# Kernel tuning notes

Hardware: AMD Instinct MI355X
Metric: run time of the kernel (lower is better)

The kernel has to match this reference:

```python
import jax, jax.numpy as jnp
import numpy as np

GEN_DIM = 200
CON_DIM = 128
CO_DIM = 4
LATENT_DIM = 64
CI_ENC_DIM = 128
EXT_DIM = 16
CLIP = 5.0
B = 65536

GEN_IN = EXT_DIM + CO_DIM            # 20
CON_IN = 2 * CI_ENC_DIM + LATENT_DIM # 320
STATE_DIM = GEN_DIM + CON_DIM + CO_DIM + CO_DIM + (CO_DIM + EXT_DIM) + LATENT_DIM  # 420


def _gru_cell(x, h, w_ih, w_hh, b_ih, b_hh, clip):
    # torch GRUCell convention: gates ordered (r, z, n), hidden clipped (LFADS ClippedGRUCell)
    gi = x @ w_ih.T + b_ih
    gh = h @ w_hh.T + b_hh
    i_r, i_z, i_n = jnp.split(gi, 3, axis=1)
    h_r, h_z, h_n = jnp.split(gh, 3, axis=1)
    r = jax.nn.sigmoid(i_r + h_r)
    z = jax.nn.sigmoid(i_z + h_z)
    n = jnp.tanh(i_n + r * h_n)
    h_new = (1.0 - z) * n + z * h
    return jnp.clip(h_new, -clip, clip)


def setup_inputs() -> dict:
    key = jax.random.key(0)
    ks = jax.random.split(key, 14)
    def w(k, shape, fan_in):
        return (jax.random.normal(k, shape, jnp.float32) / np.sqrt(fan_in)).astype(jnp.float32)
    return {
        "x": jax.random.normal(ks[0], (B, 2 * CI_ENC_DIM + EXT_DIM), jnp.float32),
        "h0": jax.random.normal(ks[1], (B, STATE_DIM), jnp.float32),
        "eps": jax.random.normal(ks[2], (B, CO_DIM), jnp.float32),
        "gen_w_ih": w(ks[3], (3 * GEN_DIM, GEN_IN), GEN_IN),
        "gen_w_hh": w(ks[4], (3 * GEN_DIM, GEN_DIM), GEN_DIM),
        "gen_b_ih": jnp.zeros((3 * GEN_DIM,), jnp.float32),
        "gen_b_hh": jnp.zeros((3 * GEN_DIM,), jnp.float32),
        "con_w_ih": w(ks[5], (3 * CON_DIM, CON_IN), CON_IN),
        "con_w_hh": w(ks[6], (3 * CON_DIM, CON_DIM), CON_DIM),
        "con_b_ih": jnp.zeros((3 * CON_DIM,), jnp.float32),
        "con_b_hh": jnp.zeros((3 * CON_DIM,), jnp.float32),
        "co_w": w(ks[7], (2 * CO_DIM, CON_DIM), CON_DIM),
        "co_b": jnp.zeros((2 * CO_DIM,), jnp.float32),
        "fac_w": w(ks[8], (LATENT_DIM, GEN_DIM), GEN_DIM),
    }


def reference(x, h0, eps, gen_w_ih, gen_w_hh, gen_b_ih, gen_b_hh,
              con_w_ih, con_w_hh, con_b_ih, con_b_hh, co_w, co_b, fac_w):
    # split h0 per state_dims [GEN, CON, CO, CO, CO+EXT, LATENT]
    o0 = GEN_DIM
    o1 = o0 + CON_DIM
    o2 = o1 + CO_DIM
    o3 = o2 + CO_DIM
    o4 = o3 + CO_DIM + EXT_DIM
    gen_state = h0[:, :o0]
    con_state = h0[:, o0:o1]
    factor = h0[:, o4:]
    # split input per [2*CI_ENC_DIM, EXT_DIM]
    ci_step = x[:, :2 * CI_ENC_DIM]
    ext_step = x[:, 2 * CI_ENC_DIM:]

    # controller path (dropout is identity at inference)
    con_input = jnp.concatenate([ci_step, factor], axis=1)
    con_state = _gru_cell(con_input, con_state, con_w_ih, con_w_hh, con_b_ih, con_b_hh, CLIP)
    co_params = con_state @ co_w.T + co_b
    co_mean = co_params[:, :CO_DIM]
    co_logvar = co_params[:, CO_DIM:]
    co_std = jnp.exp(0.5 * co_logvar)  # sqrt(exp(logvar))
    con_output = co_mean + co_std * eps  # reparameterized rsample

    gen_input = jnp.concatenate([con_output, ext_step], axis=1)
    gen_state = _gru_cell(gen_input, gen_state, gen_w_ih, gen_w_hh, gen_b_ih, gen_b_hh, CLIP)

    # kernel-normalized linear: rows L2-normalized, no bias
    normed_w = fac_w / jnp.maximum(jnp.linalg.norm(fac_w, axis=1, keepdims=True), 1e-12)
    factor = gen_state @ normed_w.T

    hidden = jnp.concatenate([gen_state, con_state, co_mean, co_std, gen_input, factor], axis=1)
    return hidden
```

## Files before the change

### kernel.cpp

```cpp
#include <hip/hip_runtime.h>
#include <math.h>


#define NT 512
#define RT 128
#define XD 272
#define HD 420

typedef unsigned short ushort_t;
typedef __attribute__((ext_vector_type(8))) short bf8;
typedef __attribute__((ext_vector_type(4))) float f4;
typedef __attribute__((ext_vector_type(4))) unsigned short us4;

#define WS_W1 0
#define WS_W2 122880
#define WS_W3 172032
#define WS_W4 191488
#define WS_W5 327680

#define STA 328
#define STG 216
#define STH 136
#define STR3 88

#define O_A   0
#define O_GN  55296
#define O_R2  83968
#define O_R3  118784
#define POOLB 141312

__device__ __forceinline__ ushort_t f2bf(float f) {
  union { float f; unsigned u; } v; v.f = f;
  unsigned r = v.u + 0x7FFFu + ((v.u >> 16) & 1u);
  return (ushort_t)(r >> 16);
}
__device__ __forceinline__ float bf2f(ushort_t u) {
  union { unsigned u; float f; } v; v.u = ((unsigned)u) << 16; return v.f;
}
__device__ __forceinline__ us4 f2bf4(f4 v) {
  us4 b; b.x = f2bf(v.x); b.y = f2bf(v.y); b.z = f2bf(v.z); b.w = f2bf(v.w); return b;
}
__device__ __forceinline__ f4 bf2f4(us4 b) {
  f4 v; v.x = bf2f(b.x); v.y = bf2f(b.y); v.z = bf2f(b.z); v.w = bf2f(b.w); return v;
}
__device__ __forceinline__ float rcpf(float x) { return __builtin_amdgcn_rcpf(x); }
__device__ __forceinline__ float sigf(float x) { return rcpf(1.0f + __expf(-x)); }
__device__ __forceinline__ float tanhf_(float x) {
  return 1.0f - 2.0f * rcpf(1.0f + __expf(2.0f * x));
}

#define MFMA(a, b, c) __builtin_amdgcn_mfma_f32_16x16x32_bf16((a), (b), (c), 0, 0, 0)

__global__ void prep_w(const float* __restrict__ cw1, const float* __restrict__ cw2,
                       const float* __restrict__ gw3, const float* __restrict__ gw4,
                       ushort_t* __restrict__ ws) {
  int tid = blockIdx.x * blockDim.x + threadIdx.x;
  int np = gridDim.x * blockDim.x;
  for (int i = tid; i < 384 * 320; i += np) ws[WS_W1 + i] = f2bf(cw1[i]);
  for (int i = tid; i < 384 * 128; i += np) ws[WS_W2 + i] = f2bf(cw2[i]);
  for (int i = tid; i < 608 * 32; i += np) {
    int n = i >> 5, k = i & 31;
    ws[WS_W3 + i] = (n < 600 && k < 20) ? f2bf(gw3[n * 20 + k]) : (ushort_t)0;
  }
  for (int i = tid; i < 608 * 224; i += np) {
    int n = i / 224, k = i - n * 224;
    ws[WS_W4 + i] = (n < 600 && k < 200) ? f2bf(gw4[n * 200 + k]) : (ushort_t)0;
  }
}

__global__ void prep_fac(const float* __restrict__ fw, ushort_t* __restrict__ ws) {
  int n = blockIdx.x;
  int l = threadIdx.x;
  float ss = 0.f;
  for (int k = l; k < 200; k += 64) { float v = fw[n * 200 + k]; ss = fmaf(v, v, ss); }
  for (int off = 32; off; off >>= 1) ss += __shfl_down(ss, off, 64);
  ss = __shfl(ss, 0, 64);
  float inv = 1.0f / fmaxf(sqrtf(ss), 1e-12f);
  for (int k = l; k < 224; k += 64)
    ws[WS_W5 + n * 224 + k] = (k < 200) ? f2bf(fw[n * 200 + k] * inv) : (ushort_t)0;
}

__global__ __launch_bounds__(NT, 2) void decoder_kernel(
    const float* __restrict__ x, const float* __restrict__ h0, const float* __restrict__ eps,
    const float* __restrict__ gen_b_ih, const float* __restrict__ gen_b_hh,
    const float* __restrict__ con_b_ih, const float* __restrict__ con_b_hh,
    const float* __restrict__ co_w, const float* __restrict__ co_b,
    const ushort_t* __restrict__ ws, float* __restrict__ out)
{
  __shared__ __align__(16) unsigned char spool[POOLB];
  ushort_t* sA  = (ushort_t*)(spool + O_A);
  ushort_t* sGo = (ushort_t*)(spool + O_A);
  ushort_t* sGn = (ushort_t*)(spool + O_GN);
  ushort_t* sR2 = (ushort_t*)(spool + O_R2);
  ushort_t* sR3 = (ushort_t*)(spool + O_R3);

  const int tid = threadIdx.x;
  const int rbase = blockIdx.x * RT;
  const int lane = tid & 63;
  const int w = tid >> 6;
  const int bn = lane & 15;
  const int kq = (lane >> 4) << 3;
  const int qrow = (lane >> 4) << 2;

  #pragma unroll
  for (int it = 0; it < 16; ++it) {
    int idx = tid + it * NT;
    int r = idx >> 6, c4 = (idx & 63) << 2;
    f4 v = *(const f4*)&x[(size_t)(rbase + r) * XD + c4];
    *(us4*)&sA[r * STA + c4] = f2bf4(v);
  }
  {
    int r = tid >> 2, e = (tid & 3) << 2;
    f4 v = *(const f4*)&x[(size_t)(rbase + r) * XD + 256 + e];
    *(us4*)&sR3[r * STR3 + 4 + e] = f2bf4(v);
    *(f4*)&out[(size_t)(rbase + r) * HD + 340 + e] = v;
  }
  #pragma unroll
  for (int it = 0; it < 8; ++it) {
    int idx = tid + it * NT;
    int r = idx >> 5, c4 = (idx & 31) << 2;
    f4 v = *(const f4*)&h0[(size_t)(rbase + r) * HD + 200 + c4];
    *(us4*)&sR2[r * STH + c4] = f2bf4(v);
  }
  #pragma unroll
  for (int it = 0; it < 4; ++it) {
    int idx = tid + it * NT;
    int r = idx >> 4, c4 = (idx & 15) << 2;
    f4 v = *(const f4*)&h0[(size_t)(rbase + r) * HD + 356 + c4];
    *(us4*)&sA[r * STA + 256 + c4] = f2bf4(v);
  }
  if (tid < 384) {
    int r = tid / 3, q = (tid - (tid / 3) * 3) << 2;
    us4 z = {0, 0, 0, 0};
    *(us4*)&sR3[r * STR3 + 20 + q] = z;
  }
  __syncthreads();

  const int col = (w << 4) + bn;

  f4 aR[8], aZ[8], aN[8], aHN[8];
  #pragma unroll
  for (int ri = 0; ri < 8; ++ri) {
    aR[ri] = (f4){0.f, 0.f, 0.f, 0.f};
    aZ[ri] = (f4){0.f, 0.f, 0.f, 0.f};
    aN[ri] = (f4){0.f, 0.f, 0.f, 0.f};
    aHN[ri] = (f4){0.f, 0.f, 0.f, 0.f};
  }
  {
    const ushort_t* W2 = ws + WS_W2;
    #pragma unroll 1
    for (int k0 = 0; k0 < 128; k0 += 32) {
      bf8 b0 = *(const bf8*)&W2[(size_t)(col) * 128 + k0 + kq];
      bf8 b1 = *(const bf8*)&W2[(size_t)(128 + col) * 128 + k0 + kq];
      bf8 bm = *(const bf8*)&W2[(size_t)(256 + col) * 128 + k0 + kq];
      #pragma unroll
      for (int ri = 0; ri < 8; ++ri) {
        bf8 a = *(const bf8*)&sR2[(ri * 16 + bn) * STH + k0 + kq];
        aR[ri] = MFMA(a, b0, aR[ri]);
        aZ[ri] = MFMA(a, b1, aZ[ri]);
        aHN[ri] = MFMA(a, bm, aHN[ri]);
      }
    }
    const ushort_t* W1 = ws + WS_W1;
    #pragma unroll 1
    for (int k0 = 0; k0 < 320; k0 += 32) {
      bf8 b0 = *(const bf8*)&W1[(size_t)(col) * 320 + k0 + kq];
      bf8 b1 = *(const bf8*)&W1[(size_t)(128 + col) * 320 + k0 + kq];
      bf8 bm = *(const bf8*)&W1[(size_t)(256 + col) * 320 + k0 + kq];
      #pragma unroll
      for (int ri = 0; ri < 8; ++ri) {
        bf8 a = *(const bf8*)&sA[(ri * 16 + bn) * STA + k0 + kq];
        aR[ri] = MFMA(a, b0, aR[ri]);
        aZ[ri] = MFMA(a, b1, aZ[ri]);
        aN[ri] = MFMA(a, bm, aN[ri]);
      }
    }
  }
  __syncthreads();

  #pragma unroll 1
  for (int idx = tid; idx < 128 * 54; idx += NT) {
    int r = idx / 54, u = idx - (idx / 54) * 54;
    if (u < 50) {
      f4 v = *(const f4*)&h0[(size_t)(rbase + r) * HD + (u << 2)];
      *(us4*)&sGo[r * STG + (u << 2)] = f2bf4(v);
    } else {
      us4 z = {0, 0, 0, 0};
      *(us4*)&sGo[r * STG + 200 + ((u - 50) << 2)] = z;
    }
  }
  {
    float brr = con_b_ih[col] + con_b_hh[col];
    float brz = con_b_ih[128 + col] + con_b_hh[128 + col];
    float bin = con_b_ih[256 + col], bhn = con_b_hh[256 + col];
    #pragma unroll
    for (int ri = 0; ri < 8; ++ri) {
      #pragma unroll
      for (int j = 0; j < 4; ++j) {
        int row = ri * 16 + qrow + j;
        float hold = bf2f(sR2[row * STH + col]);
        float rr = sigf(aR[ri][j] + brr);
        float zz = sigf(aZ[ri][j] + brz);
        float nn = tanhf_(aN[ri][j] + bin + rr * (aHN[ri][j] + bhn));
        float hv = (1.f - zz) * nn + zz * hold;
        hv = fminf(fmaxf(hv, -5.f), 5.f);
        sR2[row * STH + col] = f2bf(hv);
        out[(size_t)(rbase + row) * HD + 200 + col] = hv;
      }
    }
  }
  __syncthreads();

  {
    int cn = tid & 7;
    #pragma unroll
    for (int half = 0; half < 2; ++half) {
      int crow = (tid >> 3) + half * 64;
      float acc = co_b[cn];
      #pragma unroll 8
      for (int k0 = 0; k0 < 128; k0 += 4) {
        f4 hv = bf2f4(*(const us4*)&sR2[crow * STH + k0]);
        f4 wv = *(const f4*)&co_w[cn * 128 + k0];
        acc = fmaf(hv.x, wv.x, acc);
        acc = fmaf(hv.y, wv.y, acc);
        acc = fmaf(hv.z, wv.z, acc);
        acc = fmaf(hv.w, wv.w, acc);
      }
      float lv = __shfl(acc, lane + 4, 64);
      if (cn < 4) {
        float stdv = __expf(0.5f * lv);
        float ov = fmaf(stdv, eps[(size_t)(rbase + crow) * 4 + cn], acc);
        size_t orow = (size_t)(rbase + crow) * HD;
        out[orow + 328 + cn] = acc;
        out[orow + 332 + cn] = stdv;
        out[orow + 336 + cn] = ov;
        sR3[crow * STR3 + cn] = f2bf(ov);
      }
    }
  }
  __syncthreads();

  {
    int r = tid >> 2, q = (tid & 3) << 2;
    us4 z = {0, 0, 0, 0};
    *(us4*)&sGn[r * STG + 200 + q] = z;
  }
  {
    const ushort_t* W3 = ws + WS_W3;
    const ushort_t* W4 = ws + WS_W4;
    #pragma unroll 1
    for (int t = w; t < 13; t += 8) {
      int c = (t << 4) + bn;
      f4 gR[8], gZ[8], gN[8], gHN[8];
      #pragma unroll
      for (int ri = 0; ri < 8; ++ri) {
        gR[ri] = (f4){0.f, 0.f, 0.f, 0.f};
        gZ[ri] = (f4){0.f, 0.f, 0.f, 0.f};
        gN[ri] = (f4){0.f, 0.f, 0.f, 0.f};
        gHN[ri] = (f4){0.f, 0.f, 0.f, 0.f};
      }
      {
        bf8 b0 = *(const bf8*)&W3[(size_t)(c) * 32 + kq];
        bf8 b1 = *(const bf8*)&W3[(size_t)(200 + c) * 32 + kq];
        bf8 bm = *(const bf8*)&W3[(size_t)(400 + c) * 32 + kq];
        #pragma unroll
        for (int ri = 0; ri < 8; ++ri) {
          bf8 a = *(const bf8*)&sR3[(ri * 16 + bn) * STR3 + kq];
          gR[ri] = MFMA(a, b0, gR[ri]);
          gZ[ri] = MFMA(a, b1, gZ[ri]);
          gN[ri] = MFMA(a, bm, gN[ri]);
        }
      }
      #pragma unroll 1
      for (int k0 = 0; k0 < 224; k0 += 32) {
        bf8 b0 = *(const bf8*)&W4[(size_t)(c) * 224 + k0 + kq];
        bf8 b1 = *(const bf8*)&W4[(size_t)(200 + c) * 224 + k0 + kq];
        bf8 bm = *(const bf8*)&W4[(size_t)(400 + c) * 224 + k0 + kq];
        #pragma unroll
        for (int ri = 0; ri < 8; ++ri) {
          bf8 a = *(const bf8*)&sGo[(ri * 16 + bn) * STG + k0 + kq];
          gR[ri] = MFMA(a, b0, gR[ri]);
          gZ[ri] = MFMA(a, b1, gZ[ri]);
          gHN[ri] = MFMA(a, bm, gHN[ri]);
        }
      }
      if (c < 200) {
        float brr = gen_b_ih[c] + gen_b_hh[c];
        float brz = gen_b_ih[200 + c] + gen_b_hh[200 + c];
        float bin = gen_b_ih[400 + c], bhn = gen_b_hh[400 + c];
        #pragma unroll
        for (int ri = 0; ri < 8; ++ri) {
          #pragma unroll
          for (int j = 0; j < 4; ++j) {
            int row = ri * 16 + qrow + j;
            float hold = bf2f(sGo[row * STG + c]);
            float rr = sigf(gR[ri][j] + brr);
            float zz = sigf(gZ[ri][j] + brz);
            float nn = tanhf_(gN[ri][j] + bin + rr * (gHN[ri][j] + bhn));
            float hv = (1.f - zz) * nn + zz * hold;
            hv = fminf(fmaxf(hv, -5.f), 5.f);
            sGn[row * STG + c] = f2bf(hv);
            out[(size_t)(rbase + row) * HD + c] = hv;
          }
        }
      }
    }
  }
  __syncthreads();

  {
    const ushort_t* W5 = ws + WS_W5;
    #pragma unroll 1
    for (int job = 0; job < 4; ++job) {
      int ri = ((w & 3) << 1) + (job & 1);
      int ct = ((w >> 2) << 1) + (job >> 1);
      bf8 w5f[7];
      #pragma unroll
      for (int k = 0; k < 7; ++k)
        w5f[k] = *(const bf8*)&W5[(size_t)((ct << 4) + bn) * 224 + k * 32 + kq];
      f4 acc = (f4){0.f, 0.f, 0.f, 0.f};
      #pragma unroll
      for (int k = 0; k < 7; ++k) {
        bf8 a = *(const bf8*)&sGn[(ri * 16 + bn) * STG + k * 32 + kq];
        acc = MFMA(a, w5f[k], acc);
      }
      #pragma unroll
      for (int j = 0; j < 4; ++j) {
        int row = ri * 16 + qrow + j;
        out[(size_t)(rbase + row) * HD + 356 + (ct << 4) + bn] = acc[j];
      }
    }
  }
}

extern "C" void kernel_launch(void* const* d_in, const int* in_sizes, int n_in,
                              void* d_out, int out_size, void* d_ws, size_t ws_size,
                              hipStream_t stream) {
  const float* x        = (const float*)d_in[0];
  const float* h0       = (const float*)d_in[1];
  const float* eps      = (const float*)d_in[2];
  const float* gen_w_ih = (const float*)d_in[3];
  const float* gen_w_hh = (const float*)d_in[4];
  const float* gen_b_ih = (const float*)d_in[5];
  const float* gen_b_hh = (const float*)d_in[6];
  const float* con_w_ih = (const float*)d_in[7];
  const float* con_w_hh = (const float*)d_in[8];
  const float* con_b_ih = (const float*)d_in[9];
  const float* con_b_hh = (const float*)d_in[10];
  const float* co_w     = (const float*)d_in[11];
  const float* co_b     = (const float*)d_in[12];
  const float* fac_w    = (const float*)d_in[13];
  float* out = (float*)d_out;
  ushort_t* ws = (ushort_t*)d_ws;

  hipLaunchKernelGGL(prep_w, dim3(256), dim3(512), 0, stream,
                     con_w_ih, con_w_hh, gen_w_ih, gen_w_hh, ws);
  hipLaunchKernelGGL(prep_fac, dim3(64), dim3(64), 0, stream, fac_w, ws);

  int nrows = in_sizes[2] / 4;
  int grid = nrows / RT;
  hipLaunchKernelGGL(decoder_kernel, dim3(grid), dim3(NT), 0, stream,
                     x, h0, eps, gen_b_ih, gen_b_hh, con_b_ih, con_b_hh,
                     co_w, co_b, ws, out);
}
```

Before: 155.0 us.

## Split fused decoder into separate controller and generator kernels with 32-row tiles

Splits the single fused decoder kernel into a controller kernel and a generator kernel. The generator reads the controller output back from the output buffer in global memory. Row tiles shrink from 128 to 32 and blocks from 512 to 256 threads, which cuts shared memory per block and raises occupancy and grid size. In exchange, each weight fragment loaded from global or L2 now feeds only two row tiles instead of eight, so weight traffic per row rises. There is also an extra kernel launch and a global round trip for the generator input.

```diff
diff --git a/kernel.cpp b/kernel.cpp
--- a/kernel.cpp
+++ b/kernel.cpp
@@ -2,8 +2,6 @@
 #include <math.h>
 
 
-#define NT 512
-#define RT 128
 #define XD 272
 #define HD 420
 
@@ -21,13 +19,6 @@
 #define STA 328
 #define STG 216
 #define STH 136
-#define STR3 88
-
-#define O_A   0
-#define O_GN  55296
-#define O_R2  83968
-#define O_R3  118784
-#define POOLB 141312
 
 __device__ __forceinline__ ushort_t f2bf(float f) {
   union { float f; unsigned u; } v; v.f = f;
@@ -80,22 +71,19 @@
     ws[WS_W5 + n * 224 + k] = (k < 200) ? f2bf(fw[n * 200 + k] * inv) : (ushort_t)0;
 }
 
-__global__ __launch_bounds__(NT, 2) void decoder_kernel(
-    const float* __restrict__ x, const float* __restrict__ h0, const float* __restrict__ eps,
-    const float* __restrict__ gen_b_ih, const float* __restrict__ gen_b_hh,
+__global__ __launch_bounds__(256, 4) void con_kernel(
+    const float* __restrict__ x, const float* __restrict__ h0,
+    const float* __restrict__ eps,
     const float* __restrict__ con_b_ih, const float* __restrict__ con_b_hh,
     const float* __restrict__ co_w, const float* __restrict__ co_b,
     const ushort_t* __restrict__ ws, float* __restrict__ out)
 {
-  __shared__ __align__(16) unsigned char spool[POOLB];
-  ushort_t* sA  = (ushort_t*)(spool + O_A);
-  ushort_t* sGo = (ushort_t*)(spool + O_A);
-  ushort_t* sGn = (ushort_t*)(spool + O_GN);
-  ushort_t* sR2 = (ushort_t*)(spool + O_R2);
-  ushort_t* sR3 = (ushort_t*)(spool + O_R3);
+  __shared__ __align__(16) unsigned char spool[29696];
+  ushort_t* sA  = (ushort_t*)(spool);
+  ushort_t* sR2 = (ushort_t*)(spool + 20992);
 
   const int tid = threadIdx.x;
-  const int rbase = blockIdx.x * RT;
+  const int rbase = blockIdx.x * 32;
   const int lane = tid & 63;
   const int w = tid >> 6;
   const int bn = lane & 15;
@@ -103,83 +91,152 @@
   const int qrow = (lane >> 4) << 2;
 
   #pragma unroll
-  for (int it = 0; it < 16; ++it) {
-    int idx = tid + it * NT;
+  for (int it = 0; it < 8; ++it) {
+    int idx = tid + it * 256;
     int r = idx >> 6, c4 = (idx & 63) << 2;
     f4 v = *(const f4*)&x[(size_t)(rbase + r) * XD + c4];
     *(us4*)&sA[r * STA + c4] = f2bf4(v);
   }
-  {
+  if (tid < 128) {
     int r = tid >> 2, e = (tid & 3) << 2;
     f4 v = *(const f4*)&x[(size_t)(rbase + r) * XD + 256 + e];
-    *(us4*)&sR3[r * STR3 + 4 + e] = f2bf4(v);
     *(f4*)&out[(size_t)(rbase + r) * HD + 340 + e] = v;
   }
   #pragma unroll
-  for (int it = 0; it < 8; ++it) {
-    int idx = tid + it * NT;
+  for (int it = 0; it < 4; ++it) {
+    int idx = tid + it * 256;
     int r = idx >> 5, c4 = (idx & 31) << 2;
     f4 v = *(const f4*)&h0[(size_t)(rbase + r) * HD + 200 + c4];
     *(us4*)&sR2[r * STH + c4] = f2bf4(v);
   }
   #pragma unroll
-  for (int it = 0; it < 4; ++it) {
-    int idx = tid + it * NT;
+  for (int it = 0; it < 2; ++it) {
+    int idx = tid + it * 256;
     int r = idx >> 4, c4 = (idx & 15) << 2;
     f4 v = *(const f4*)&h0[(size_t)(rbase + r) * HD + 356 + c4];
     *(us4*)&sA[r * STA + 256 + c4] = f2bf4(v);
   }
-  if (tid < 384) {
-    int r = tid / 3, q = (tid - (tid / 3) * 3) << 2;
-    us4 z = {0, 0, 0, 0};
-    *(us4*)&sR3[r * STR3 + 20 + q] = z;
-  }
-  __syncthreads();
-
-  const int col = (w << 4) + bn;
-
-  f4 aR[8], aZ[8], aN[8], aHN[8];
-  #pragma unroll
-  for (int ri = 0; ri < 8; ++ri) {
-    aR[ri] = (f4){0.f, 0.f, 0.f, 0.f};
-    aZ[ri] = (f4){0.f, 0.f, 0.f, 0.f};
-    aN[ri] = (f4){0.f, 0.f, 0.f, 0.f};
-    aHN[ri] = (f4){0.f, 0.f, 0.f, 0.f};
-  }
-  {
+  __syncthreads();
+
+  f4 aR[2][2], aZ[2][2], aN[2][2], aHN[2][2];
+  #pragma unroll
+  for (int ti = 0; ti < 2; ++ti)
+    #pragma unroll
+    for (int rt = 0; rt < 2; ++rt) {
+      aR[ti][rt] = (f4){0.f, 0.f, 0.f, 0.f};
+      aZ[ti][rt] = (f4){0.f, 0.f, 0.f, 0.f};
+      aN[ti][rt] = (f4){0.f, 0.f, 0.f, 0.f};
+      aHN[ti][rt] = (f4){0.f, 0.f, 0.f, 0.f};
+    }
+  #pragma unroll
+  for (int ti = 0; ti < 2; ++ti) {
+    const int col = ((w + 4 * ti) << 4) + bn;
     const ushort_t* W2 = ws + WS_W2;
-    #pragma unroll 1
+    #pragma unroll
     for (int k0 = 0; k0 < 128; k0 += 32) {
       bf8 b0 = *(const bf8*)&W2[(size_t)(col) * 128 + k0 + kq];
       bf8 b1 = *(const bf8*)&W2[(size_t)(128 + col) * 128 + k0 + kq];
       bf8 bm = *(const bf8*)&W2[(size_t)(256 + col) * 128 + k0 + kq];
       #pragma unroll
-      for (int ri = 0; ri < 8; ++ri) {
-        bf8 a = *(const bf8*)&sR2[(ri * 16 + bn) * STH + k0 + kq];
-        aR[ri] = MFMA(a, b0, aR[ri]);
-        aZ[ri] = MFMA(a, b1, aZ[ri]);
-        aHN[ri] = MFMA(a, bm, aHN[ri]);
+      for (int rt = 0; rt < 2; ++rt) {
+        bf8 a = *(const bf8*)&sR2[(rt * 16 + bn) * STH + k0 + kq];
+        aR[ti][rt] = MFMA(a, b0, aR[ti][rt]);
+        aZ[ti][rt] = MFMA(a, b1, aZ[ti][rt]);
+        aHN[ti][rt] = MFMA(a, bm, aHN[ti][rt]);
       }
     }
     const ushort_t* W1 = ws + WS_W1;
-    #pragma unroll 1
+    #pragma unroll
     for (int k0 = 0; k0 < 320; k0 += 32) {
       bf8 b0 = *(const bf8*)&W1[(size_t)(col) * 320 + k0 + kq];
       bf8 b1 = *(const bf8*)&W1[(size_t)(128 + col) * 320 + k0 + kq];
       bf8 bm = *(const bf8*)&W1[(size_t)(256 + col) * 320 + k0 + kq];
       #pragma unroll
-      for (int ri = 0; ri < 8; ++ri) {
-        bf8 a = *(const bf8*)&sA[(ri * 16 + bn) * STA + k0 + kq];
-        aR[ri] = MFMA(a, b0, aR[ri]);
-        aZ[ri] = MFMA(a, b1, aZ[ri]);
-        aN[ri] = MFMA(a, bm, aN[ri]);
-      }
-    }
-  }
-  __syncthreads();
-
-  #pragma unroll 1
-  for (int idx = tid; idx < 128 * 54; idx += NT) {
+      for (int rt = 0; rt < 2; ++rt) {
+        bf8 a = *(const bf8*)&sA[(rt * 16 + bn) * STA + k0 + kq];
+        aR[ti][rt] = MFMA(a, b0, aR[ti][rt]);
+        aZ[ti][rt] = MFMA(a, b1, aZ[ti][rt]);
+        aN[ti][rt] = MFMA(a, bm, aN[ti][rt]);
+      }
+    }
+  }
+  __syncthreads();
+
+  #pragma unroll
+  for (int ti = 0; ti < 2; ++ti) {
+    const int col = ((w + 4 * ti) << 4) + bn;
+    float brr = con_b_ih[col] + con_b_hh[col];
+    float brz = con_b_ih[128 + col] + con_b_hh[128 + col];
+    float bin = con_b_ih[256 + col], bhn = con_b_hh[256 + col];
+    #pragma unroll
+    for (int rt = 0; rt < 2; ++rt) {
+      #pragma unroll
+      for (int j = 0; j < 4; ++j) {
+        int row = rt * 16 + qrow + j;
+        float hold = bf2f(sR2[row * STH + col]);
+        float rr = sigf(aR[ti][rt][j] + brr);
+        float zz = sigf(aZ[ti][rt][j] + brz);
+        float nn = tanhf_(aN[ti][rt][j] + bin + rr * (aHN[ti][rt][j] + bhn));
+        float hv = (1.f - zz) * nn + zz * hold;
+        hv = fminf(fmaxf(hv, -5.f), 5.f);
+        sR2[row * STH + col] = f2bf(hv);
+        out[(size_t)(rbase + row) * HD + 200 + col] = hv;
+      }
+    }
+  }
+  __syncthreads();
+
+  {
+    int crow = tid >> 3, cn = tid & 7;
+    float acc = co_b[cn];
+    #pragma unroll 8
+    for (int k0 = 0; k0 < 128; k0 += 4) {
+      f4 hv = bf2f4(*(const us4*)&sR2[crow * STH + k0]);
+      f4 wv = *(const f4*)&co_w[cn * 128 + k0];
+      acc = fmaf(hv.x, wv.x, acc);
+      acc = fmaf(hv.y, wv.y, acc);
+      acc = fmaf(hv.z, wv.z, acc);
+      acc = fmaf(hv.w, wv.w, acc);
+    }
+    float lv = __shfl(acc, lane + 4, 64);
+    if (cn < 4) {
+      float stdv = __expf(0.5f * lv);
+      float ov = fmaf(stdv, eps[(size_t)(rbase + crow) * 4 + cn], acc);
+      size_t orow = (size_t)(rbase + crow) * HD;
+      out[orow + 328 + cn] = acc;
+      out[orow + 332 + cn] = stdv;
+      out[orow + 336 + cn] = ov;
+    }
+  }
+}
+
+__global__ __launch_bounds__(256, 4) void gen_kernel(
+    const float* __restrict__ h0,
+    const float* __restrict__ gen_b_ih, const float* __restrict__ gen_b_hh,
+    const ushort_t* __restrict__ ws, float* out)
+{
+  __shared__ __align__(16) unsigned char spool[29696];
+  ushort_t* sGo = (ushort_t*)(spool);
+  ushort_t* sGn = (ushort_t*)(spool + 13824);
+  ushort_t* sGI = (ushort_t*)(spool + 27648);
+
+  const int tid = threadIdx.x;
+  const int rbase = blockIdx.x * 32;
+  const int lane = tid & 63;
+  const int w = tid >> 6;
+  const int bn = lane & 15;
+  const int kq = (lane >> 4) << 3;
+  const int qrow = (lane >> 4) << 2;
+
+  #pragma unroll
+  for (int it = 0; it < 7; ++it) {
+    int idx = tid + it * 256;
+    if (idx < 1728) {
+      us4 z = {0, 0, 0, 0};
+      *(us4*)&sGn[idx << 2] = z;
+    }
+  }
+  for (int idx = tid; idx < 32 * 54; idx += 256) {
     int r = idx / 54, u = idx - (idx / 54) * 54;
     if (u < 50) {
       f4 v = *(const f4*)&h0[(size_t)(rbase + r) * HD + (u << 2)];
@@ -189,99 +246,56 @@
       *(us4*)&sGo[r * STG + 200 + ((u - 50) << 2)] = z;
     }
   }
-  {
-    float brr = con_b_ih[col] + con_b_hh[col];
-    float brz = con_b_ih[128 + col] + con_b_hh[128 + col];
-    float bin = con_b_ih[256 + col], bhn = con_b_hh[256 + col];
-    #pragma unroll
-    for (int ri = 0; ri < 8; ++ri) {
-      #pragma unroll
-      for (int j = 0; j < 4; ++j) {
-        int row = ri * 16 + qrow + j;
-        float hold = bf2f(sR2[row * STH + col]);
-        float rr = sigf(aR[ri][j] + brr);
-        float zz = sigf(aZ[ri][j] + brz);
-        float nn = tanhf_(aN[ri][j] + bin + rr * (aHN[ri][j] + bhn));
-        float hv = (1.f - zz) * nn + zz * hold;
-        hv = fminf(fmaxf(hv, -5.f), 5.f);
-        sR2[row * STH + col] = f2bf(hv);
-        out[(size_t)(rbase + row) * HD + 200 + col] = hv;
-      }
-    }
-  }
-  __syncthreads();
-
-  {
-    int cn = tid & 7;
-    #pragma unroll
-    for (int half = 0; half < 2; ++half) {
-      int crow = (tid >> 3) + half * 64;
-      float acc = co_b[cn];
-      #pragma unroll 8
-      for (int k0 = 0; k0 < 128; k0 += 4) {
-        f4 hv = bf2f4(*(const us4*)&sR2[crow * STH + k0]);
-        f4 wv = *(const f4*)&co_w[cn * 128 + k0];
-        acc = fmaf(hv.x, wv.x, acc);
-        acc = fmaf(hv.y, wv.y, acc);
-        acc = fmaf(hv.z, wv.z, acc);
-        acc = fmaf(hv.w, wv.w, acc);
-      }
-      float lv = __shfl(acc, lane + 4, 64);
-      if (cn < 4) {
-        float stdv = __expf(0.5f * lv);
-        float ov = fmaf(stdv, eps[(size_t)(rbase + crow) * 4 + cn], acc);
-        size_t orow = (size_t)(rbase + crow) * HD;
-        out[orow + 328 + cn] = acc;
-        out[orow + 332 + cn] = stdv;
-        out[orow + 336 + cn] = ov;
-        sR3[crow * STR3 + cn] = f2bf(ov);
-      }
-    }
-  }
-  __syncthreads();
-
-  {
-    int r = tid >> 2, q = (tid & 3) << 2;
-    us4 z = {0, 0, 0, 0};
-    *(us4*)&sGn[r * STG + 200 + q] = z;
-  }
+  if (tid < 160) {
+    int r = tid / 5, q = tid - (tid / 5) * 5;
+    f4 v = *(const f4*)&out[(size_t)(rbase + r) * HD + 336 + (q << 2)];
+    *(us4*)&sGI[r * 32 + (q << 2)] = f2bf4(v);
+  } else if (tid < 256) {
+    int t2 = tid - 160;
+    if (t2 < 96) {
+      int r = t2 / 3, q3 = t2 - (t2 / 3) * 3;
+      us4 z = {0, 0, 0, 0};
+      *(us4*)&sGI[r * 32 + 20 + (q3 << 2)] = z;
+    }
+  }
+  __syncthreads();
+
   {
     const ushort_t* W3 = ws + WS_W3;
     const ushort_t* W4 = ws + WS_W4;
-    #pragma unroll 1
-    for (int t = w; t < 13; t += 8) {
+    for (int t = w; t < 13; t += 4) {
       int c = (t << 4) + bn;
-      f4 gR[8], gZ[8], gN[8], gHN[8];
-      #pragma unroll
-      for (int ri = 0; ri < 8; ++ri) {
-        gR[ri] = (f4){0.f, 0.f, 0.f, 0.f};
-        gZ[ri] = (f4){0.f, 0.f, 0.f, 0.f};
-        gN[ri] = (f4){0.f, 0.f, 0.f, 0.f};
-        gHN[ri] = (f4){0.f, 0.f, 0.f, 0.f};
+      f4 gR[2], gZ[2], gN[2], gHN[2];
+      #pragma unroll
+      for (int rt = 0; rt < 2; ++rt) {
+        gR[rt] = (f4){0.f, 0.f, 0.f, 0.f};
+        gZ[rt] = (f4){0.f, 0.f, 0.f, 0.f};
+        gN[rt] = (f4){0.f, 0.f, 0.f, 0.f};
+        gHN[rt] = (f4){0.f, 0.f, 0.f, 0.f};
       }
       {
         bf8 b0 = *(const bf8*)&W3[(size_t)(c) * 32 + kq];
         bf8 b1 = *(const bf8*)&W3[(size_t)(200 + c) * 32 + kq];
         bf8 bm = *(const bf8*)&W3[(size_t)(400 + c) * 32 + kq];
         #pragma unroll
-        for (int ri = 0; ri < 8; ++ri) {
-          bf8 a = *(const bf8*)&sR3[(ri * 16 + bn) * STR3 + kq];
-          gR[ri] = MFMA(a, b0, gR[ri]);
-          gZ[ri] = MFMA(a, b1, gZ[ri]);
-          gN[ri] = MFMA(a, bm, gN[ri]);
+        for (int rt = 0; rt < 2; ++rt) {
+          bf8 a = *(const bf8*)&sGI[(rt * 16 + bn) * 32 + kq];
+          gR[rt] = MFMA(a, b0, gR[rt]);
+          gZ[rt] = MFMA(a, b1, gZ[rt]);
+          gN[rt] = MFMA(a, bm, gN[rt]);
         }
       }
-      #pragma unroll 1
+      #pragma unroll
       for (int k0 = 0; k0 < 224; k0 += 32) {
         bf8 b0 = *(const bf8*)&W4[(size_t)(c) * 224 + k0 + kq];
         bf8 b1 = *(const bf8*)&W4[(size_t)(200 + c) * 224 + k0 + kq];
         bf8 bm = *(const bf8*)&W4[(size_t)(400 + c) * 224 + k0 + kq];
         #pragma unroll
-        for (int ri = 0; ri < 8; ++ri) {
-          bf8 a = *(const bf8*)&sGo[(ri * 16 + bn) * STG + k0 + kq];
-          gR[ri] = MFMA(a, b0, gR[ri]);
-          gZ[ri] = MFMA(a, b1, gZ[ri]);
-          gHN[ri] = MFMA(a, bm, gHN[ri]);
+        for (int rt = 0; rt < 2; ++rt) {
+          bf8 a = *(const bf8*)&sGo[(rt * 16 + bn) * STG + k0 + kq];
+          gR[rt] = MFMA(a, b0, gR[rt]);
+          gZ[rt] = MFMA(a, b1, gZ[rt]);
+          gHN[rt] = MFMA(a, bm, gHN[rt]);
         }
       }
       if (c < 200) {
@@ -289,14 +303,14 @@
         float brz = gen_b_ih[200 + c] + gen_b_hh[200 + c];
         float bin = gen_b_ih[400 + c], bhn = gen_b_hh[400 + c];
         #pragma unroll
-        for (int ri = 0; ri < 8; ++ri) {
+        for (int rt = 0; rt < 2; ++rt) {
           #pragma unroll
           for (int j = 0; j < 4; ++j) {
-            int row = ri * 16 + qrow + j;
+            int row = rt * 16 + qrow + j;
             float hold = bf2f(sGo[row * STG + c]);
-            float rr = sigf(gR[ri][j] + brr);
-            float zz = sigf(gZ[ri][j] + brz);
-            float nn = tanhf_(gN[ri][j] + bin + rr * (gHN[ri][j] + bhn));
+            float rr = sigf(gR[rt][j] + brr);
+            float zz = sigf(gZ[rt][j] + brz);
+            float nn = tanhf_(gN[rt][j] + bin + rr * (gHN[rt][j] + bhn));
             float hv = (1.f - zz) * nn + zz * hold;
             hv = fminf(fmaxf(hv, -5.f), 5.f);
             sGn[row * STG + c] = f2bf(hv);
@@ -310,23 +324,20 @@
 
   {
     const ushort_t* W5 = ws + WS_W5;
-    #pragma unroll 1
-    for (int job = 0; job < 4; ++job) {
-      int ri = ((w & 3) << 1) + (job & 1);
-      int ct = ((w >> 2) << 1) + (job >> 1);
-      bf8 w5f[7];
-      #pragma unroll
-      for (int k = 0; k < 7; ++k)
-        w5f[k] = *(const bf8*)&W5[(size_t)((ct << 4) + bn) * 224 + k * 32 + kq];
+    int rt = w & 1;
+    #pragma unroll
+    for (int cc = 0; cc < 2; ++cc) {
+      int ct = (w >> 1) + 2 * cc;
       f4 acc = (f4){0.f, 0.f, 0.f, 0.f};
       #pragma unroll
-      for (int k = 0; k < 7; ++k) {
-        bf8 a = *(const bf8*)&sGn[(ri * 16 + bn) * STG + k * 32 + kq];
-        acc = MFMA(a, w5f[k], acc);
+      for (int k0 = 0; k0 < 224; k0 += 32) {
+        bf8 b = *(const bf8*)&W5[(size_t)((ct << 4) + bn) * 224 + k0 + kq];
+        bf8 a = *(const bf8*)&sGn[(rt * 16 + bn) * STG + k0 + kq];
+        acc = MFMA(a, b, acc);
       }
       #pragma unroll
       for (int j = 0; j < 4; ++j) {
-        int row = ri * 16 + qrow + j;
+        int row = rt * 16 + qrow + j;
         out[(size_t)(rbase + row) * HD + 356 + (ct << 4) + bn] = acc[j];
       }
     }
@@ -358,8 +369,9 @@
   hipLaunchKernelGGL(prep_fac, dim3(64), dim3(64), 0, stream, fac_w, ws);
 
   int nrows = in_sizes[2] / 4;
-  int grid = nrows / RT;
-  hipLaunchKernelGGL(decoder_kernel, dim3(grid), dim3(NT), 0, stream,
-                     x, h0, eps, gen_b_ih, gen_b_hh, con_b_ih, con_b_hh,
-                     co_w, co_b, ws, out);
-}
+  int grid = nrows / 32;
+  hipLaunchKernelGGL(con_kernel, dim3(grid), dim3(256), 0, stream,
+                     x, h0, eps, con_b_ih, con_b_hh, co_w, co_b, ws, out);
+  hipLaunchKernelGGL(gen_kernel, dim3(grid), dim3(256), 0, stream,
+                     h0, gen_b_ih, gen_b_hh, ws, out);
+}
```

New measurement: 216.2 us. 39.5% more time.
